# Kernel optimization log

Hardware: AMD Instinct MI355X
Metric: run time of the kernel (lower is better)

## Reference

```python
import jax, jax.numpy as jnp
import numpy as np

B, T, K = 32, 64, 5
VOCAB, DE, DA, DI, H = 32000, 300, 300, 2048, 512


def setup_inputs() -> dict:
    key = jax.random.key(0)
    ks = jax.random.split(key, 8)
    return {
        'top_k_attributes': jax.random.randint(ks[0], (B, K), 0, 1000, dtype=jnp.int32),
        'mean_image_features': jax.random.normal(ks[1], (B, DI), jnp.float32),
        'seq_inputs': jax.random.randint(ks[2], (B, T), 0, VOCAB, dtype=jnp.int32),
        'lengths': jax.random.randint(ks[3], (B,), 1, T + 1, dtype=jnp.int32),
        'word_emb': jax.random.normal(ks[4], (VOCAB, DE), jnp.float32) * 0.02,
        'attr_emb': jax.random.normal(ks[5], (1000, DA), jnp.float32) * 0.02,
        'lstm_kernel': jax.random.normal(ks[6], (DE + DI + DA + H, 4 * H), jnp.float32) * 0.02,
        'lstm_bias': jnp.zeros((4 * H,), jnp.float32),
        'W_logits': jax.random.normal(ks[7], (H, VOCAB), jnp.float32) * 0.02,
        'b_logits': jnp.zeros((VOCAB,), jnp.float32),
    }


def reference(top_k_attributes, mean_image_features, seq_inputs, lengths,
              word_emb, attr_emb, lstm_kernel, lstm_bias, W_logits, b_logits):
    # attribute features: lookup + mean over the K attributes
    attr_feats = attr_emb[top_k_attributes]              # [B,K,DA]
    mean_attr = attr_feats.mean(axis=1)                  # [B,DA]
    feats = jnp.concatenate([mean_image_features, mean_attr], axis=-1)  # [B,DI+DA]

    x = word_emb[seq_inputs]                             # [B,T,DE]
    # per-step cell input = concat(word_emb_t, image+attr features)
    inp = jnp.concatenate([x, jnp.broadcast_to(feats[:, None, :], (B, T, feats.shape[-1]))], axis=-1)

    def step(carry, x_t):
        h, c = carry
        z = jnp.concatenate([x_t, h], axis=-1) @ lstm_kernel + lstm_bias  # [B,4H]
        i, f, g, o = jnp.split(z, 4, axis=-1)
        c = jax.nn.sigmoid(f) * c + jax.nn.sigmoid(i) * jnp.tanh(g)
        h = jax.nn.sigmoid(o) * jnp.tanh(c)
        return (h, c), h

    h0 = jnp.zeros((B, H), inp.dtype)
    (_, _), h_seq = jax.lax.scan(step, (h0, h0), jnp.transpose(inp, (1, 0, 2)))
    h_seq = jnp.transpose(h_seq, (1, 0, 2))              # [B,T,H]

    # dynamic_rnn zeros activations past each sequence length
    mask = (jnp.arange(T)[None, :] < lengths[:, None])[:, :, None]
    h_seq = jnp.where(mask, h_seq, 0.0)

    logits = jnp.einsum('bth,hv->btv', h_seq, W_logits) + b_logits  # [B,T,V]
    return logits, jnp.argmax(logits, axis=-1).astype(jnp.int32)
```

## Files before the change

### kernel.cpp

```cpp
#include <hip/hip_runtime.h>
#include <hip/hip_bf16.h>
#include <math.h>

#define BATCH 32
#define TSEQ  64
#define KATTR 5
#define VOCAB 32000
#define DE    300
#define DA    300
#define DI    2048
#define HDIM  512
#define G4    2048
#define WOFF  (DE + DI + DA)

__global__ void zero_kernel(float* __restrict__ p, int n) {
    int i = blockIdx.x * blockDim.x + threadIdx.x;
    if (i < n) p[i] = 0.f;
}

__global__ void mean_attr_kernel(const int* __restrict__ topk,
                                 const float* __restrict__ attr_emb,
                                 float* __restrict__ mean_attr) {
    int b = blockIdx.x;
    int tid = threadIdx.x;
    if (tid < DA) {
        float s = 0.f;
        #pragma unroll
        for (int q = 0; q < KATTR; ++q) {
            int a = topk[b * KATTR + q];
            s += attr_emb[(size_t)a * DA + tid];
        }
        mean_attr[b * DA + tid] = s / (float)KATTR;
    }
}

__launch_bounds__(256)
__global__ void zf_kernel(const float* __restrict__ img,
                          const float* __restrict__ mean_attr,
                          const float* __restrict__ Wk,
                          const float* __restrict__ bias,
                          float* __restrict__ zf) {
    int b = blockIdx.y;
    int j = blockIdx.x * 256 + threadIdx.x;
    float acc = bias[j];
    const float* wimg = Wk + (size_t)DE * G4 + j;
    const float* irow = img + b * DI;
    #pragma unroll 8
    for (int k = 0; k < DI; ++k) acc += irow[k] * wimg[(size_t)k * G4];
    const float* wattr = Wk + (size_t)(DE + DI) * G4 + j;
    const float* arow = mean_attr + b * DA;
    #pragma unroll 4
    for (int k = 0; k < DA; ++k) acc += arow[k] * wattr[(size_t)k * G4];
    zf[b * G4 + j] = acc;
}

__launch_bounds__(256)
__global__ void whr_kernel(const float* __restrict__ Wk, float* __restrict__ Whr) {
    const int bid = blockIdx.x;
    const int tid = threadIdx.x;
    for (int it = 0; it < 16; ++it) {
        int Q = it * 256 + tid;
        int k = Q >> 3, jj = Q & 7;
        int g = jj >> 1, p = jj & 1;
        Whr[(size_t)bid * 4096 + Q] = Wk[(size_t)(WOFF + k) * G4 + g * HDIM + bid * 2 + p];
    }
}

template<bool GATHER, bool PERROW>
__launch_bounds__(256)
__global__ void gemm_tile(const float* __restrict__ A,
                          const int* __restrict__ gidx,
                          const float* __restrict__ Bm,
                          const float* __restrict__ addv,
                          float* __restrict__ C,
                          int M, int N, int K, int lda) {
    __shared__ __align__(16) float As[16][68];
    __shared__ __align__(16) float Bs[16][68];
    const int tid = threadIdx.x;
    const int n0 = blockIdx.x * 64;
    const int m0 = blockIdx.y * 64;
    const int tx = tid & 15, ty = tid >> 4;
    const int ar  = tid >> 2;
    const int akq = (tid & 3) << 2;
    const int bkr = tid >> 4;
    const int bc  = (tid & 15) << 2;

    size_t arow;
    if (GATHER) arow = (size_t)gidx[m0 + ar] * (size_t)lda;
    else        arow = (size_t)(m0 + ar) * (size_t)lda;

    float a00=0,a01=0,a02=0,a03=0, a10=0,a11=0,a12=0,a13=0;
    float a20=0,a21=0,a22=0,a23=0, a30=0,a31=0,a32=0,a33=0;

    for (int k0 = 0; k0 < K; k0 += 16) {
        int ka = k0 + akq;
        float4 av;
        if (ka + 4 <= K) {
            av = *(const float4*)(A + arow + ka);
        } else {
            av.x = (ka + 0 < K) ? A[arow + ka + 0] : 0.f;
            av.y = (ka + 1 < K) ? A[arow + ka + 1] : 0.f;
            av.z = (ka + 2 < K) ? A[arow + ka + 2] : 0.f;
            av.w = (ka + 3 < K) ? A[arow + ka + 3] : 0.f;
        }
        As[akq + 0][ar] = av.x;
        As[akq + 1][ar] = av.y;
        As[akq + 2][ar] = av.z;
        As[akq + 3][ar] = av.w;

        int kb = k0 + bkr;
        float4 bv;
        if (kb < K) bv = *(const float4*)(Bm + (size_t)kb * N + n0 + bc);
        else { bv.x = bv.y = bv.z = bv.w = 0.f; }
        *(float4*)&Bs[bkr][bc] = bv;

        __syncthreads();
        #pragma unroll
        for (int kk = 0; kk < 16; ++kk) {
            const float4 a4 = *(const float4*)&As[kk][ty << 2];
            const float4 b4 = *(const float4*)&Bs[kk][tx << 2];
            a00 += a4.x * b4.x; a01 += a4.x * b4.y; a02 += a4.x * b4.z; a03 += a4.x * b4.w;
            a10 += a4.y * b4.x; a11 += a4.y * b4.y; a12 += a4.y * b4.z; a13 += a4.y * b4.w;
            a20 += a4.z * b4.x; a21 += a4.z * b4.y; a22 += a4.z * b4.z; a23 += a4.z * b4.w;
            a30 += a4.w * b4.x; a31 += a4.w * b4.y; a32 += a4.w * b4.z; a33 += a4.w * b4.w;
        }
        __syncthreads();
    }

    float accs[4][4] = {{a00,a01,a02,a03},{a10,a11,a12,a13},{a20,a21,a22,a23},{a30,a31,a32,a33}};
    const int n = n0 + (tx << 2);
    #pragma unroll
    for (int i = 0; i < 4; ++i) {
        int m = m0 + (ty << 2) + i;
        const float* av2 = PERROW ? (addv + (size_t)(m >> 6) * N) : addv;
        float4 o;
        o.x = accs[i][0] + av2[n + 0];
        o.y = accs[i][1] + av2[n + 1];
        o.z = accs[i][2] + av2[n + 2];
        o.w = accs[i][3] + av2[n + 3];
        *(float4*)(C + (size_t)m * N + n) = o;
    }
}

__global__ void build_rows(const int* __restrict__ lengths,
                           int* __restrict__ rowlist, int* __restrict__ mact) {
    __shared__ int len[BATCH];
    __shared__ int off[BATCH + 1];
    int tid = threadIdx.x;
    if (tid < BATCH) len[tid] = lengths[tid];
    __syncthreads();
    if (tid == 0) {
        int s = 0;
        for (int b = 0; b < BATCH; ++b) { off[b] = s; s += len[b]; }
        off[BATCH] = s;
        *mact = s;
    }
    __syncthreads();
    int total = off[BATCH];
    for (int i = tid; i < BATCH * TSEQ; i += 256) {
        int b = i >> 6, t = i & 63;
        if (t < len[b]) rowlist[off[b] + t] = i;
    }
    for (int i = tid; i < BATCH * TSEQ; i += 256) {
        if (i >= total) rowlist[i] = 0;
    }
}

__launch_bounds__(256, 1)
__global__ void lstm_step2(const float* __restrict__ z_pre,
                           const float* __restrict__ Whr,
                           const float* __restrict__ hin,
                           float* __restrict__ hout,
                           float* __restrict__ cbuf,
                           float* __restrict__ h_seq,
                           const int* __restrict__ lengths,
                           int t) {
    __shared__ __align__(16) float hsT[HDIM][36];
    __shared__ __align__(16) float wsm[HDIM][12];
    __shared__ __align__(16) float zp[16 * 260];
    __shared__ float zfull[BATCH][8];
    const int bid = blockIdx.x;
    const int tid = threadIdx.x;

    float zp4[4] = {0, 0, 0, 0};
    int glen = 0, gb = 0, gkk = 0;
    float c_old = 0.f;
    if (tid < 64) {
        gb = tid & 31;
        int kp = tid >> 5;
        gkk = bid * 2 + kp;
        glen = lengths[gb];
        const float* zr = z_pre + ((size_t)(gb * TSEQ + t)) * G4 + gkk;
        zp4[0] = zr[0 * HDIM];
        zp4[1] = zr[1 * HDIM];
        zp4[2] = zr[2 * HDIM];
        zp4[3] = zr[3 * HDIM];
        c_old = cbuf[gkk * BATCH + gb];
    }

    #pragma unroll
    for (int it = 0; it < 16; ++it) {
        int Q = it * 256 + tid;
        int k = Q >> 3, bq = Q & 7;
        float4 v = *(const float4*)(hin + (size_t)Q * 4);
        *(float4*)&hsT[k][bq * 4] = v;
    }
    const float* wsrc = Whr + (size_t)bid * 4096;
    #pragma unroll
    for (int it = 0; it < 4; ++it) {
        int Q = it * 256 + tid;
        int k = Q >> 1, jjq = Q & 1;
        float4 v = *(const float4*)(wsrc + (size_t)Q * 4);
        *(float4*)&wsm[k][jjq * 4] = v;
    }
    __syncthreads();

    {
        const int kseg = tid >> 4;
        const int tile = tid & 15;
        const int b0 = (tile >> 1) << 2;
        const int j0 = (tile & 1) << 2;
        const int kb = kseg << 5;
        float a00=0,a01=0,a02=0,a03=0, a10=0,a11=0,a12=0,a13=0;
        float a20=0,a21=0,a22=0,a23=0, a30=0,a31=0,a32=0,a33=0;
        #pragma unroll 8
        for (int kk = 0; kk < 32; ++kk) {
            const int k = kb + kk;
            const float4 h4 = *(const float4*)&hsT[k][b0];
            const float4 w4 = *(const float4*)&wsm[k][j0];
            a00 += h4.x * w4.x; a01 += h4.x * w4.y; a02 += h4.x * w4.z; a03 += h4.x * w4.w;
            a10 += h4.y * w4.x; a11 += h4.y * w4.y; a12 += h4.y * w4.z; a13 += h4.y * w4.w;
            a20 += h4.z * w4.x; a21 += h4.z * w4.y; a22 += h4.z * w4.z; a23 += h4.z * w4.w;
            a30 += h4.w * w4.x; a31 += h4.w * w4.y; a32 += h4.w * w4.z; a33 += h4.w * w4.w;
        }
        float* zpr = &zp[kseg * 260 + tile * 16];
        *(float4*)(zpr + 0)  = make_float4(a00, a01, a02, a03);
        *(float4*)(zpr + 4)  = make_float4(a10, a11, a12, a13);
        *(float4*)(zpr + 8)  = make_float4(a20, a21, a22, a23);
        *(float4*)(zpr + 12) = make_float4(a30, a31, a32, a33);
    }
    __syncthreads();

    {
        const int b = tid & 31, jj = tid >> 5;
        const int tile2 = ((b >> 2) << 1) + (jj >> 2);
        const int e = ((b & 3) << 2) + (jj & 3);
        float s = 0.f;
        #pragma unroll
        for (int ks = 0; ks < 16; ++ks) s += zp[ks * 260 + tile2 * 16 + e];
        zfull[b][jj] = s;
    }
    __syncthreads();

    if (tid < 64) {
        const int kp = tid >> 5;
        float zi = zfull[gb][0 * 2 + kp] + zp4[0];
        float zF = zfull[gb][1 * 2 + kp] + zp4[1];
        float zg = zfull[gb][2 * 2 + kp] + zp4[2];
        float zo = zfull[gb][3 * 2 + kp] + zp4[3];
        float si = 1.f / (1.f + expf(-zi));
        float sf = 1.f / (1.f + expf(-zF));
        float so = 1.f / (1.f + expf(-zo));
        float c_new = sf * c_old + si * tanhf(zg);
        float h_new = so * tanhf(c_new);
        cbuf[gkk * BATCH + gb] = c_new;
        hout[gkk * BATCH + gb] = h_new;
        h_seq[((size_t)(gb * TSEQ + t)) * HDIM + gkk] = (t < glen) ? h_new : 0.f;
    }
}

__launch_bounds__(256)
__global__ void fill_masked(const int* __restrict__ lengths,
                            const float* __restrict__ blog,
                            float* __restrict__ logits) {
    int row = blockIdx.x;
    int b = row >> 6, t = row & 63;
    if (t < lengths[b]) return;
    float* p = logits + (size_t)row * VOCAB;
    for (int v = threadIdx.x * 4; v < VOCAB; v += 256 * 4) {
        float4 o;
        o.x = blog[v + 0]; o.y = blog[v + 1]; o.z = blog[v + 2]; o.w = blog[v + 3];
        *(float4*)(p + v) = o;
    }
}

__launch_bounds__(256)
__global__ void gemm_logits(const float* __restrict__ A,
                            const int* __restrict__ rowlist,
                            const int* __restrict__ mactp,
                            const float* __restrict__ Bm,
                            const float* __restrict__ blog,
                            float* __restrict__ C) {
    const int Mact = *mactp;
    const int m0 = blockIdx.y * 64;
    if (m0 >= Mact) return;
    __shared__ __align__(16) float As[16][68];
    __shared__ __align__(16) float Bs[16][68];
    const int tid = threadIdx.x;
    const int n0 = blockIdx.x * 64;
    const int tx = tid & 15, ty = tid >> 4;
    const int ar  = tid >> 2;
    const int akq = (tid & 3) << 2;
    const int bkr = tid >> 4;
    const int bc  = (tid & 15) << 2;
    const int K = HDIM, N = VOCAB;

    size_t arow = (size_t)rowlist[m0 + ar] * (size_t)HDIM;

    float a00=0,a01=0,a02=0,a03=0, a10=0,a11=0,a12=0,a13=0;
    float a20=0,a21=0,a22=0,a23=0, a30=0,a31=0,a32=0,a33=0;

    for (int k0 = 0; k0 < K; k0 += 16) {
        float4 av = *(const float4*)(A + arow + k0 + akq);
        As[akq + 0][ar] = av.x;
        As[akq + 1][ar] = av.y;
        As[akq + 2][ar] = av.z;
        As[akq + 3][ar] = av.w;
        float4 bv = *(const float4*)(Bm + (size_t)(k0 + bkr) * N + n0 + bc);
        *(float4*)&Bs[bkr][bc] = bv;
        __syncthreads();
        #pragma unroll
        for (int kk = 0; kk < 16; ++kk) {
            const float4 a4 = *(const float4*)&As[kk][ty << 2];
            const float4 b4 = *(const float4*)&Bs[kk][tx << 2];
            a00 += a4.x * b4.x; a01 += a4.x * b4.y; a02 += a4.x * b4.z; a03 += a4.x * b4.w;
            a10 += a4.y * b4.x; a11 += a4.y * b4.y; a12 += a4.y * b4.z; a13 += a4.y * b4.w;
            a20 += a4.z * b4.x; a21 += a4.z * b4.y; a22 += a4.z * b4.z; a23 += a4.z * b4.w;
            a30 += a4.w * b4.x; a31 += a4.w * b4.y; a32 += a4.w * b4.z; a33 += a4.w * b4.w;
        }
        __syncthreads();
    }

    float accs[4][4] = {{a00,a01,a02,a03},{a10,a11,a12,a13},{a20,a21,a22,a23},{a30,a31,a32,a33}};
    const int n = n0 + (tx << 2);
    #pragma unroll
    for (int i = 0; i < 4; ++i) {
        int m = m0 + (ty << 2) + i;
        if (m < Mact) {
            int rm = rowlist[m];
            float4 o;
            o.x = accs[i][0] + blog[n + 0];
            o.y = accs[i][1] + blog[n + 1];
            o.z = accs[i][2] + blog[n + 2];
            o.w = accs[i][3] + blog[n + 3];
            *(float4*)(C + (size_t)rm * VOCAB + n) = o;
        }
    }
}

__launch_bounds__(256)
__global__ void argmax_kernel(const float* __restrict__ logits, float* __restrict__ outa) {
    const int row = blockIdx.x;
    const int tid = threadIdx.x;
    const float* p = logits + (size_t)row * VOCAB;
    float bv = -INFINITY; int bi = VOCAB;
    for (int v = tid; v < VOCAB; v += 256) {
        float x = p[v];
        if (x > bv) { bv = x; bi = v; }
    }
    __shared__ float sv[256];
    __shared__ int   si[256];
    sv[tid] = bv; si[tid] = bi;
    __syncthreads();
    for (int s = 128; s > 0; s >>= 1) {
        if (tid < s) {
            if (sv[tid + s] > sv[tid] || (sv[tid + s] == sv[tid] && si[tid + s] < si[tid])) {
                sv[tid] = sv[tid + s]; si[tid] = si[tid + s];
            }
        }
        __syncthreads();
    }
    if (tid == 0) outa[row] = (float)si[0];
}

extern "C" void kernel_launch(void* const* d_in, const int* in_sizes, int n_in,
                              void* d_out, int out_size, void* d_ws, size_t ws_size,
                              hipStream_t stream) {
    const int*   topk     = (const int*)d_in[0];
    const float* img      = (const float*)d_in[1];
    const int*   seq      = (const int*)d_in[2];
    const int*   lengths  = (const int*)d_in[3];
    const float* word_emb = (const float*)d_in[4];
    const float* attr_emb = (const float*)d_in[5];
    const float* Wk       = (const float*)d_in[6];
    const float* bias     = (const float*)d_in[7];
    const float* Wlog     = (const float*)d_in[8];
    const float* blog     = (const float*)d_in[9];

    float* out_logits = (float*)d_out;
    float* out_argmax = out_logits + (size_t)BATCH * TSEQ * VOCAB;

    float* ws        = (float*)d_ws;
    float* mean_attr = ws;
    float* zf        = mean_attr + BATCH * DA;
    float* cbuf      = zf + BATCH * G4;
    float* hb0       = cbuf + HDIM * BATCH;
    float* hb1       = hb0 + HDIM * BATCH;
    float* h_seq     = hb1 + HDIM * BATCH;
    float* Whr       = h_seq + (size_t)BATCH * TSEQ * HDIM;
    int*   rowlist   = (int*)(Whr + (size_t)256 * 4096);
    int*   mact      = rowlist + BATCH * TSEQ;
    float* z_pre     = out_logits;

    zero_kernel<<<dim3((2 * HDIM * BATCH + 255) / 256), 256, 0, stream>>>(cbuf, 2 * HDIM * BATCH);

    build_rows<<<1, 256, 0, stream>>>(lengths, rowlist, mact);

    whr_kernel<<<dim3(256), 256, 0, stream>>>(Wk, Whr);

    mean_attr_kernel<<<dim3(BATCH), 320, 0, stream>>>(topk, attr_emb, mean_attr);

    zf_kernel<<<dim3(G4 / 256, BATCH), 256, 0, stream>>>(img, mean_attr, Wk, bias, zf);

    gemm_tile<true, true><<<dim3(G4 / 64, (BATCH * TSEQ) / 64), 256, 0, stream>>>(
        word_emb, seq, Wk, zf, z_pre, BATCH * TSEQ, G4, DE, DE);

    float* hin = hb0;
    float* hout = hb1;
    for (int t = 0; t < TSEQ; ++t) {
        lstm_step2<<<dim3(256), 256, 0, stream>>>(z_pre, Whr, hin, hout, cbuf, h_seq, lengths, t);
        float* tmp = hin; hin = hout; hout = tmp;
    }

    fill_masked<<<dim3(BATCH * TSEQ), 256, 0, stream>>>(lengths, blog, out_logits);

    gemm_logits<<<dim3(VOCAB / 64, (BATCH * TSEQ) / 64), 256, 0, stream>>>(
        h_seq, rowlist, mact, Wlog, blog, out_logits);

    argmax_kernel<<<dim3(BATCH * TSEQ), 256, 0, stream>>>(out_logits, out_argmax);
}
```

Before: 1.450 ms.

## Enlarge logits GEMM tile to 128x128 with XCD-aware block remapping

Replaces the 64x64-tile output-projection GEMM with a 128x128 tile, where each thread computes an 8x8 micro-tile split into four 4x4 quadrants. This raises arithmetic intensity per shared-memory load and per global fetch of W_logits. It also switches to a 1D grid with block-index swizzling ((bid&7)*chunk + bid>>3), so consecutive tiles land on the same XCD for better L2 reuse. The cost is more registers per thread (64 accumulators), which may lower occupancy, and coarser early exit when the active row count is not a multiple of 128.

```diff
diff --git a/kernel.cpp b/kernel.cpp
--- a/kernel.cpp
+++ b/kernel.cpp
@@ -285,65 +285,100 @@
 }
 
 __launch_bounds__(256)
-__global__ void gemm_logits(const float* __restrict__ A,
-                            const int* __restrict__ rowlist,
-                            const int* __restrict__ mactp,
-                            const float* __restrict__ Bm,
-                            const float* __restrict__ blog,
-                            float* __restrict__ C) {
+__global__ void gemm_logits128(const float* __restrict__ A,
+                               const int* __restrict__ rowlist,
+                               const int* __restrict__ mactp,
+                               const float* __restrict__ Bm,
+                               const float* __restrict__ blog,
+                               float* __restrict__ C) {
     const int Mact = *mactp;
-    const int m0 = blockIdx.y * 64;
+    const int chunk = gridDim.x >> 3;
+    const int L = (blockIdx.x & 7) * chunk + (blockIdx.x >> 3);
+    const int m0 = (L & 15) * 128;
+    const int n0 = (L >> 4) * 128;
     if (m0 >= Mact) return;
-    __shared__ __align__(16) float As[16][68];
-    __shared__ __align__(16) float Bs[16][68];
+
+    __shared__ __align__(16) float As[16][132];
+    __shared__ __align__(16) float Bs[16][132];
     const int tid = threadIdx.x;
-    const int n0 = blockIdx.x * 64;
     const int tx = tid & 15, ty = tid >> 4;
-    const int ar  = tid >> 2;
+
+    const int am  = tid >> 2;
     const int akq = (tid & 3) << 2;
-    const int bkr = tid >> 4;
-    const int bc  = (tid & 15) << 2;
-    const int K = HDIM, N = VOCAB;
-
-    size_t arow = (size_t)rowlist[m0 + ar] * (size_t)HDIM;
-
-    float a00=0,a01=0,a02=0,a03=0, a10=0,a11=0,a12=0,a13=0;
-    float a20=0,a21=0,a22=0,a23=0, a30=0,a31=0,a32=0,a33=0;
-
-    for (int k0 = 0; k0 < K; k0 += 16) {
-        float4 av = *(const float4*)(A + arow + k0 + akq);
-        As[akq + 0][ar] = av.x;
-        As[akq + 1][ar] = av.y;
-        As[akq + 2][ar] = av.z;
-        As[akq + 3][ar] = av.w;
-        float4 bv = *(const float4*)(Bm + (size_t)(k0 + bkr) * N + n0 + bc);
-        *(float4*)&Bs[bkr][bc] = bv;
+    const size_t arow0 = (size_t)rowlist[m0 + am]      * HDIM;
+    const size_t arow1 = (size_t)rowlist[m0 + 64 + am] * HDIM;
+    const int bk = tid >> 5;
+    const int bc = (tid & 31) << 2;
+
+    float c00[4][4] = {}, c01[4][4] = {}, c10[4][4] = {}, c11[4][4] = {};
+
+    for (int k0 = 0; k0 < HDIM; k0 += 16) {
+        const float4 av0 = *(const float4*)(A + arow0 + k0 + akq);
+        const float4 av1 = *(const float4*)(A + arow1 + k0 + akq);
+        As[akq + 0][am] = av0.x;
+        As[akq + 1][am] = av0.y;
+        As[akq + 2][am] = av0.z;
+        As[akq + 3][am] = av0.w;
+        As[akq + 0][64 + am] = av1.x;
+        As[akq + 1][64 + am] = av1.y;
+        As[akq + 2][64 + am] = av1.z;
+        As[akq + 3][64 + am] = av1.w;
+        const float4 bv0 = *(const float4*)(Bm + (size_t)(k0 + bk)     * VOCAB + n0 + bc);
+        const float4 bv1 = *(const float4*)(Bm + (size_t)(k0 + 8 + bk) * VOCAB + n0 + bc);
+        *(float4*)&Bs[bk][bc]     = bv0;
+        *(float4*)&Bs[bk + 8][bc] = bv1;
         __syncthreads();
         #pragma unroll
         for (int kk = 0; kk < 16; ++kk) {
-            const float4 a4 = *(const float4*)&As[kk][ty << 2];
-            const float4 b4 = *(const float4*)&Bs[kk][tx << 2];
-            a00 += a4.x * b4.x; a01 += a4.x * b4.y; a02 += a4.x * b4.z; a03 += a4.x * b4.w;
-            a10 += a4.y * b4.x; a11 += a4.y * b4.y; a12 += a4.y * b4.z; a13 += a4.y * b4.w;
-            a20 += a4.z * b4.x; a21 += a4.z * b4.y; a22 += a4.z * b4.z; a23 += a4.z * b4.w;
-            a30 += a4.w * b4.x; a31 += a4.w * b4.y; a32 += a4.w * b4.z; a33 += a4.w * b4.w;
+            const float4 aL = *(const float4*)&As[kk][ty << 2];
+            const float4 aH = *(const float4*)&As[kk][64 + (ty << 2)];
+            const float4 bL = *(const float4*)&Bs[kk][tx << 2];
+            const float4 bH = *(const float4*)&Bs[kk][64 + (tx << 2)];
+            const float a_[8] = {aL.x, aL.y, aL.z, aL.w, aH.x, aH.y, aH.z, aH.w};
+            const float b_[8] = {bL.x, bL.y, bL.z, bL.w, bH.x, bH.y, bH.z, bH.w};
+            #pragma unroll
+            for (int i = 0; i < 4; ++i) {
+                #pragma unroll
+                for (int j = 0; j < 4; ++j) {
+                    c00[i][j] += a_[i]     * b_[j];
+                    c01[i][j] += a_[i]     * b_[4 + j];
+                    c10[i][j] += a_[4 + i] * b_[j];
+                    c11[i][j] += a_[4 + i] * b_[4 + j];
+                }
+            }
         }
         __syncthreads();
     }
 
-    float accs[4][4] = {{a00,a01,a02,a03},{a10,a11,a12,a13},{a20,a21,a22,a23},{a30,a31,a32,a33}};
-    const int n = n0 + (tx << 2);
+    const int nL = n0 + (tx << 2);
+    const int nH = nL + 64;
+    const float4 gL = *(const float4*)(blog + nL);
+    const float4 gH = *(const float4*)(blog + nH);
+    const float gLa[4] = {gL.x, gL.y, gL.z, gL.w};
+    const float gHa[4] = {gH.x, gH.y, gH.z, gH.w};
     #pragma unroll
     for (int i = 0; i < 4; ++i) {
-        int m = m0 + (ty << 2) + i;
-        if (m < Mact) {
-            int rm = rowlist[m];
-            float4 o;
-            o.x = accs[i][0] + blog[n + 0];
-            o.y = accs[i][1] + blog[n + 1];
-            o.z = accs[i][2] + blog[n + 2];
-            o.w = accs[i][3] + blog[n + 3];
-            *(float4*)(C + (size_t)rm * VOCAB + n) = o;
+        const int mL = m0 + (ty << 2) + i;
+        if (mL < Mact) {
+            const size_t rm = (size_t)rowlist[mL] * VOCAB;
+            float4 oL, oH;
+            oL.x = c00[i][0] + gLa[0]; oL.y = c00[i][1] + gLa[1];
+            oL.z = c00[i][2] + gLa[2]; oL.w = c00[i][3] + gLa[3];
+            oH.x = c01[i][0] + gHa[0]; oH.y = c01[i][1] + gHa[1];
+            oH.z = c01[i][2] + gHa[2]; oH.w = c01[i][3] + gHa[3];
+            *(float4*)(C + rm + nL) = oL;
+            *(float4*)(C + rm + nH) = oH;
+        }
+        const int mH = mL + 64;
+        if (mH < Mact) {
+            const size_t rm = (size_t)rowlist[mH] * VOCAB;
+            float4 oL, oH;
+            oL.x = c10[i][0] + gLa[0]; oL.y = c10[i][1] + gLa[1];
+            oL.z = c10[i][2] + gLa[2]; oL.w = c10[i][3] + gLa[3];
+            oH.x = c11[i][0] + gHa[0]; oH.y = c11[i][1] + gHa[1];
+            oH.z = c11[i][2] + gHa[2]; oH.w = c11[i][3] + gHa[3];
+            *(float4*)(C + rm + nL) = oL;
+            *(float4*)(C + rm + nH) = oH;
         }
     }
 }
@@ -424,7 +459,7 @@
 
     fill_masked<<<dim3(BATCH * TSEQ), 256, 0, stream>>>(lengths, blog, out_logits);
 
-    gemm_logits<<<dim3(VOCAB / 64, (BATCH * TSEQ) / 64), 256, 0, stream>>>(
+    gemm_logits128<<<dim3((VOCAB / 128) * ((BATCH * TSEQ) / 128)), 256, 0, stream>>>(
         h_seq, rowlist, mact, Wlog, blog, out_logits);
 
     argmax_kernel<<<dim3(BATCH * TSEQ), 256, 0, stream>>>(out_logits, out_argmax);
```

Result: faster. 1.408 ms (-2.9%).
